# Optimization experiments

Hardware: AMD Instinct MI355X
Metric: run time of the kernel (lower is better)

Reference implementation:

```python
import jax, jax.numpy as jnp
import numpy as np

N_NODES = 100000
IN_FEAT = 128
HIDDEN = 256
OUT = 2
N_EDGES = 600000
EPS = 1e-12  # F.normalize eps


def glorot(key, shape):
    fan_in, fan_out = shape[1], shape[0]
    lim = jnp.sqrt(6.0 / (fan_in + fan_out))
    return jax.random.uniform(key, shape, jnp.float32, -lim, lim)


def setup_inputs() -> dict:
    key = jax.random.key(0)
    ks = jax.random.split(key, 8)
    x = jax.random.normal(ks[0], (N_NODES, IN_FEAT), jnp.float32)
    edge_index = jax.random.randint(ks[1], (2, N_EDGES), 0, N_NODES, jnp.int64)
    return {
        'x': x,
        'edge_index': edge_index,
        'W1_l': glorot(ks[2], (HIDDEN, IN_FEAT)),
        'b1': jnp.zeros((HIDDEN,), jnp.float32),
        'W1_r': glorot(ks[3], (HIDDEN, IN_FEAT)),
        'W2_l': glorot(ks[4], (OUT, HIDDEN)),
        'b2': jnp.zeros((OUT,), jnp.float32),
        'W2_r': glorot(ks[5], (OUT, HIDDEN)),
    }


def sage_conv(x, src, dst, W_l, b_l, W_r):
    # mean aggregation of neighbor (source) features onto destination nodes
    msgs = x[src]  # [E, d]
    s = jax.ops.segment_sum(msgs, dst, num_segments=N_NODES)
    cnt = jax.ops.segment_sum(jnp.ones((src.shape[0], 1), x.dtype), dst,
                              num_segments=N_NODES)
    agg = s / jnp.maximum(cnt, 1.0)  # nodes with no in-edges stay 0
    out = agg @ W_l.T + b_l + x @ W_r.T  # lin_l(agg) + lin_r(x)
    # L2 normalize (normalize=True in SAGEConv)
    nrm = jnp.linalg.norm(out, axis=-1, keepdims=True)
    return out / jnp.maximum(nrm, EPS)


def reference(x, edge_index, W1_l, b1, W1_r, W2_l, b2, W2_r):
    src, dst = edge_index[0], edge_index[1]
    h = sage_conv(x, src, dst, W1_l, b1, W1_r)
    h = jax.nn.relu(h)
    # dropout(p=0.2) is identity in eval mode
    h = sage_conv(h, src, dst, W2_l, b2, W2_r)
    return jax.nn.log_softmax(h, axis=1)
```

## Files before the change

kernel.cpp:

```cpp
#include <hip/hip_runtime.h>
#include <hip/hip_fp16.h>

#define NN  100000
#define FIN 128
#define HID 256
#define NE  600000
#define FEPS 1e-12f


typedef _Float16 f16x8 __attribute__((ext_vector_type(8)));
typedef float    f32x4 __attribute__((ext_vector_type(4)));

__device__ __forceinline__ int clampN(int v) {
    return ((unsigned)v < (unsigned)NN) ? v : 0;
}
__device__ __forceinline__ int detect4(const int* ei) {
    return ((ei[1] | ei[3] | ei[5] | ei[7]) == 0) ? 1 : 0;
}
__device__ __forceinline__ int ld_src(const int* ei, int e, int f) {
    return f ? ei[2 * e] : ei[e];
}
__device__ __forceinline__ int ld_dst(const int* ei, int e, int f) {
    return f ? ei[2 * (NE + e)] : ei[NE + e];
}

__device__ __forceinline__ unsigned packh2(__half a, __half b) {
    return __builtin_bit_cast(unsigned, __halves2half2(a, b));
}

__device__ __forceinline__ int offAt(const int* __restrict__ off,
                                     const int* __restrict__ bsum, int i) {
    return (i < NN) ? (off[i] + bsum[i >> 10]) : NE;
}

__device__ __forceinline__ size_t fragIdx(int j, int k) {
    return ((size_t)((k >> 5) * 16 + (j >> 4)) * 64 +
            (size_t)(((k >> 3) & 3) * 16 + (j & 15))) * 8 + (k & 7);
}

__global__ __launch_bounds__(256) void setup_kernel(
    const int* __restrict__ ei,
    const float* __restrict__ x,
    const float* __restrict__ W1l, const float* __restrict__ W1r,
    __half* __restrict__ Bfh, __half* __restrict__ Bfl,
    __half* __restrict__ xh,
    int* __restrict__ cnt, int ncv)
{
    int b = blockIdx.x;
    int t = threadIdx.x;
    if (b < 256) {
        int j = b, k2 = t;
        float v = (k2 < FIN) ? W1l[(size_t)j * FIN + k2]
                             : W1r[(size_t)j * FIN + (k2 - FIN)];
        __half h  = __float2half_rn(v);
        __half lo = __float2half_rn(v - __half2float(h));
        size_t fi = fragIdx(j, k2);
        Bfh[fi] = h;
        Bfl[fi] = lo;
    } else if (b < 256 + ncv) {
        int idx = (b - 256) * 256 + t;
        if (idx < NN * FIN / 8) {
            const float4* px = (const float4*)(x + (size_t)idx * 8);
            float4 v0 = px[0], v1 = px[1];
            uint4 u;
            u.x = packh2(__float2half_rn(v0.x), __float2half_rn(v0.y));
            u.y = packh2(__float2half_rn(v0.z), __float2half_rn(v0.w));
            u.z = packh2(__float2half_rn(v1.x), __float2half_rn(v1.y));
            u.w = packh2(__float2half_rn(v1.z), __float2half_rn(v1.w));
            ((uint4*)xh)[idx] = u;
        }
    } else {
        int e = (b - 256 - ncv) * 256 + t;
        if (e < NE) {
            int f = detect4(ei);
            atomicAdd(cnt + clampN(ld_dst(ei, e, f)), 1);
        }
    }
}

__global__ __launch_bounds__(1024) void scan_kernel(
    const int* __restrict__ cnt, int* __restrict__ off, int* bsum,
    int* flag, int nblocks)
{
    __shared__ int sm[1024];
    __shared__ int amLast;
    int t = threadIdx.x;
    int idx = blockIdx.x * 1024 + t;
    int v = (idx < NN) ? cnt[idx] : 0;
    sm[t] = v;
    __syncthreads();
    for (int d = 1; d < 1024; d <<= 1) {
        int w = (t >= d) ? sm[t - d] : 0;
        __syncthreads();
        sm[t] += w;
        __syncthreads();
    }
    if (idx < NN) off[idx] = sm[t] - v;
    if (t == 1023) {
        bsum[blockIdx.x] = sm[1023];
        __threadfence();
        amLast = (atomicAdd(flag, 1) == nblocks - 1);
    }
    __syncthreads();
    if (amLast) {
        volatile int* vb = (volatile int*)bsum;
        int bv = (t < nblocks) ? vb[t] : 0;
        __syncthreads();
        sm[t] = (t < 128) ? ((t < nblocks) ? bv : 0) : 0;
        __syncthreads();
        for (int d = 1; d < 128; d <<= 1) {
            int w2 = (t >= d && t < 128) ? sm[t - d] : 0;
            __syncthreads();
            if (t < 128) sm[t] += w2;
            __syncthreads();
        }
        if (t < nblocks) bsum[t] = sm[t] - bv;
    }
}

__global__ __launch_bounds__(256) void fill_kernel(
    const int* __restrict__ ei,
    const int* __restrict__ off, const int* __restrict__ bsum,
    int* __restrict__ cur, int* __restrict__ col)
{
    int e = blockIdx.x * 256 + threadIdx.x;
    if (e >= NE) return;
    int f = detect4(ei);
    int src = clampN(ld_src(ei, e, f));
    int dst = clampN(ld_dst(ei, e, f));
    int p = atomicAdd(cur + dst, 1);
    col[offAt(off, bsum, dst) + p] = src;
}

__global__ __launch_bounds__(256) void gather_kernel(
    const int* __restrict__ off, const int* __restrict__ bsum,
    const int* __restrict__ col,
    const __half* __restrict__ xh,
    __half* __restrict__ aggH, __half* __restrict__ aggL)
{
    int wid = (blockIdx.x * 256 + threadIdx.x) >> 6;
    if (wid >= NN) return;
    const int n     = wid;
    const int l     = threadIdx.x & 63;
    const int ft    = l & 15;
    const int e     = l >> 4;
    const int fbase = ft * 8;

    float a[8];
#pragma unroll
    for (int i = 0; i < 8; ++i) a[i] = 0.0f;

    const int s0 = offAt(off, bsum, n);
    const int s1 = offAt(off, bsum, n + 1);

    for (int i = s0 + e; i < s1; i += 4) {
        int c = clampN(col[i]);
        uint4 v = *(const uint4*)(xh + (size_t)c * FIN + fbase);
#pragma unroll
        for (int u = 0; u < 4; ++u) {
            float2 f0 = __half22float2(__builtin_bit_cast(__half2, (&v.x)[u]));
            a[2 * u]     += f0.x;
            a[2 * u + 1] += f0.y;
        }
    }
#pragma unroll
    for (int k = 0; k < 8; ++k) {
        a[k] += __shfl_xor(a[k], 16);
        a[k] += __shfl_xor(a[k], 32);
    }

    if (e == 0) {
        float ic = 1.0f / fmaxf((float)(s1 - s0), 1.0f);
        __half h[8], lo[8];
#pragma unroll
        for (int k = 0; k < 8; ++k) {
            float v = a[k] * ic;
            h[k]  = __float2half_rn(v);
            lo[k] = __float2half_rn(v - __half2float(h[k]));
        }
        uint4 uh, ul;
        uh.x = packh2(h[0], h[1]);   uh.y = packh2(h[2], h[3]);
        uh.z = packh2(h[4], h[5]);   uh.w = packh2(h[6], h[7]);
        ul.x = packh2(lo[0], lo[1]); ul.y = packh2(lo[2], lo[3]);
        ul.z = packh2(lo[4], lo[5]); ul.w = packh2(lo[6], lo[7]);
        size_t rowb = (size_t)n * 128 + (size_t)((ft ^ (n & 7)) << 3);
        *(uint4*)(aggH + rowb) = uh;
        *(uint4*)(aggL + rowb) = ul;
    }
}

__device__ __forceinline__ void splitStore4(
    __half* Ah, __half* Al, int addr, float4 v)
{
    __half h0 = __float2half_rn(v.x), h1 = __float2half_rn(v.y);
    __half h2 = __float2half_rn(v.z), h3 = __float2half_rn(v.w);
    __half l0 = __float2half_rn(v.x - __half2float(h0));
    __half l1 = __float2half_rn(v.y - __half2float(h1));
    __half l2 = __float2half_rn(v.z - __half2float(h2));
    __half l3 = __float2half_rn(v.w - __half2float(h3));
    uint2 uh, ul;
    uh.x = packh2(h0, h1);  uh.y = packh2(h2, h3);
    ul.x = packh2(l0, l1);  ul.y = packh2(l2, l3);
    *(uint2*)(Ah + addr) = uh;
    *(uint2*)(Al + addr) = ul;
}

__device__ __forceinline__ void mfma_phase(
    const __half* Ah, const __half* Al,
    const __half* __restrict__ Bfh, const __half* __restrict__ Bfl,
    int pb , int baseA0, int baseA1, int r7,
    int jg0, int l, f32x4 acc[2][4])
{
    const int kg = l >> 4;
#pragma unroll
    for (int kk = 0; kk < 4; ++kk) {
        const int chunk = kk * 4 + kg;
        const int sl = (chunk ^ r7) << 3;
        f16x8 ah0 = *reinterpret_cast<const f16x8*>(Ah + baseA0 + sl);
        f16x8 al0 = *reinterpret_cast<const f16x8*>(Al + baseA0 + sl);
        f16x8 ah1 = *reinterpret_cast<const f16x8*>(Ah + baseA1 + sl);
        f16x8 al1 = *reinterpret_cast<const f16x8*>(Al + baseA1 + sl);
#pragma unroll
        for (int jt = 0; jt < 4; ++jt) {
            const size_t bo = (((size_t)(pb + kk) * 16 + jg0 + jt) * 64 + l) * 8;
            f16x8 bh = *reinterpret_cast<const f16x8*>(Bfh + bo);
            f16x8 bl = *reinterpret_cast<const f16x8*>(Bfl + bo);
            acc[0][jt] = __builtin_amdgcn_mfma_f32_16x16x32_f16(ah0, bh, acc[0][jt], 0, 0, 0);
            acc[1][jt] = __builtin_amdgcn_mfma_f32_16x16x32_f16(ah1, bh, acc[1][jt], 0, 0, 0);
            acc[0][jt] = __builtin_amdgcn_mfma_f32_16x16x32_f16(al0, bh, acc[0][jt], 0, 0, 0);
            acc[1][jt] = __builtin_amdgcn_mfma_f32_16x16x32_f16(al1, bh, acc[1][jt], 0, 0, 0);
            acc[0][jt] = __builtin_amdgcn_mfma_f32_16x16x32_f16(ah0, bl, acc[0][jt], 0, 0, 0);
            acc[1][jt] = __builtin_amdgcn_mfma_f32_16x16x32_f16(ah1, bl, acc[1][jt], 0, 0, 0);
        }
    }
}

__global__ __launch_bounds__(512, 4) void gemm_mfma_kernel(
    const __half* __restrict__ aggH, const __half* __restrict__ aggL,
    const float* __restrict__ x,
    const __half* __restrict__ Bfh, const __half* __restrict__ Bfl,
    const float* __restrict__ b1,
    const float* __restrict__ W2l, const float* __restrict__ W2r,
    float* __restrict__ g, float* __restrict__ r)
{
    __shared__ __half Ah[64 * 128];
    __shared__ __half Al[64 * 128];

    const int t  = threadIdx.x;
    const int nb = blockIdx.x * 64;

    {
        const uint4* gh = (const uint4*)(aggH + (size_t)nb * 128);
        const uint4* gl = (const uint4*)(aggL + (size_t)nb * 128);
#pragma unroll
        for (int i = 0; i < 2; ++i) {
            int idx = i * 512 + t;
            *(uint4*)(Ah + idx * 8) = gh[idx];
            *(uint4*)(Al + idx * 8) = gl[idx];
        }
    }
    __syncthreads();

    const int l     = t & 63;
    const int w     = t >> 6;
    const int ln    = l & 15;
    const int kg    = l >> 4;
    const int mrow0 = (w & 1) * 32;
    const int jg0   = (w >> 1) * 4;

    f32x4 acc[2][4];
#pragma unroll
    for (int mt = 0; mt < 2; ++mt)
#pragma unroll
        for (int jt = 0; jt < 4; ++jt)
            acc[mt][jt] = (f32x4){0.f, 0.f, 0.f, 0.f};

    const int rowA0  = mrow0 + ln;
    const int rowA1  = mrow0 + 16 + ln;
    const int baseA0 = rowA0 * 128;
    const int baseA1 = rowA1 * 128;
    const int r7     = ln & 7;

    mfma_phase(Ah, Al, Bfh, Bfl, 0, baseA0, baseA1, r7, jg0, l, acc);
    __syncthreads();

    {
        const float4* xF = (const float4*)x;
        const float4 z4 = make_float4(0.f, 0.f, 0.f, 0.f);
#pragma unroll
        for (int i = 0; i < 4; ++i) {
            int idx   = i * 512 + t;
            int n_loc = idx >> 5;
            int kq    = idx & 31;
            int n     = nb + n_loc;
            float4 v  = (n < NN) ? xF[(size_t)n * 32 + kq] : z4;
            int addr  = n_loc * 128 + ((((kq >> 1) ^ (n_loc & 7)) << 3) | ((kq & 1) << 2));
            splitStore4(Ah, Al, addr, v);
        }
    }
    __syncthreads();

    mfma_phase(Ah, Al, Bfh, Bfl, 4, baseA0, baseA1, r7, jg0, l, acc);

    const int jb2 = jg0 * 16;
    float b1v[4], wl0[4], wl1[4], wr0[4], wr1[4];
#pragma unroll
    for (int jt = 0; jt < 4; ++jt) {
        int j = jb2 + jt * 16 + ln;
        b1v[jt] = b1[j];
        wl0[jt] = W2l[j];        wl1[jt] = W2l[HID + j];
        wr0[jt] = W2r[j];        wr1[jt] = W2r[HID + j];
    }

    __syncthreads();
    float* red = (float*)Ah;
#pragma unroll
    for (int mt = 0; mt < 2; ++mt) {
#pragma unroll
        for (int rg = 0; rg < 4; ++rg) {
            float s = 0.f, G0 = 0.f, G1 = 0.f, R0 = 0.f, R1 = 0.f;
#pragma unroll
            for (int jt = 0; jt < 4; ++jt) {
                float oo = acc[mt][jt][rg] + b1v[jt];
                s = fmaf(oo, oo, s);
                float pp = fmaxf(oo, 0.f);
                G0 = fmaf(pp, wl0[jt], G0);
                G1 = fmaf(pp, wl1[jt], G1);
                R0 = fmaf(pp, wr0[jt], R0);
                R1 = fmaf(pp, wr1[jt], R1);
            }
#pragma unroll
            for (int m = 1; m < 16; m <<= 1) {
                s  += __shfl_xor(s, m);
                G0 += __shfl_xor(G0, m);
                G1 += __shfl_xor(G1, m);
                R0 += __shfl_xor(R0, m);
                R1 += __shfl_xor(R1, m);
            }
            if (ln == 0) {
                int n_loc = mrow0 + mt * 16 + kg * 4 + rg;
                float* pp = red + ((size_t)(w >> 1) * 64 + n_loc) * 5;
                pp[0] = s;  pp[1] = G0; pp[2] = G1; pp[3] = R0; pp[4] = R1;
            }
        }
    }
    __syncthreads();

    if (t < 64) {
        int n = nb + t;
        if (n < NN) {
            float s = 0.f, G0 = 0.f, G1 = 0.f, R0 = 0.f, R1 = 0.f;
#pragma unroll
            for (int jg = 0; jg < 4; ++jg) {
                const float* pp = red + ((size_t)jg * 64 + t) * 5;
                s += pp[0]; G0 += pp[1]; G1 += pp[2]; R0 += pp[3]; R1 += pp[4];
            }
            float inv = 1.0f / fmaxf(sqrtf(s), FEPS);
            g[2 * (size_t)n]     = G0 * inv;
            g[2 * (size_t)n + 1] = G1 * inv;
            r[2 * (size_t)n]     = R0 * inv;
            r[2 * (size_t)n + 1] = R1 * inv;
        }
    }
}

__device__ __forceinline__ void phaseB_epilogue(
    float* smem_f, int t, int l, int nb,
    const __half* __restrict__ Bfh, const __half* __restrict__ Bfl,
    const float* __restrict__ b1,
    const float* __restrict__ W2l, const float* __restrict__ W2r,
    float* __restrict__ g, float* __restrict__ r)
{
    const int w  = __builtin_amdgcn_readfirstlane(t >> 6);
    const int jb = w * 16;

    float o[16];
#pragma unroll
    for (int i = 0; i < 16; ++i) o[i] = 0.0f;

#pragma unroll 1
    for (int k2 = 0; k2 < 2 * FIN; k2 += 4) {
        const int nc = l ^ ((k2 >> 3) & 31);
        float av0 = smem_f[(k2 + 0) * 64 + nc];
        float av1 = smem_f[(k2 + 1) * 64 + nc];
        float av2 = smem_f[(k2 + 2) * 64 + nc];
        float av3 = smem_f[(k2 + 3) * 64 + nc];
#pragma unroll
        for (int i = 0; i < 16; ++i) {
            const size_t fb = ((size_t)((k2 >> 5) * 16 + ((jb + i) >> 4)) * 64 +
                               (size_t)(((k2 >> 3) & 3) * 16 + ((jb + i) & 15))) * 8 +
                              (k2 & 7);
            const __half* ph = Bfh + fb;
            const __half* pl = Bfl + fb;
            float oi = o[i];
            oi = fmaf(av0, __half2float(ph[0]) + __half2float(pl[0]), oi);
            oi = fmaf(av1, __half2float(ph[1]) + __half2float(pl[1]), oi);
            oi = fmaf(av2, __half2float(ph[2]) + __half2float(pl[2]), oi);
            oi = fmaf(av3, __half2float(ph[3]) + __half2float(pl[3]), oi);
            o[i] = oi;
        }
    }

    float sq = 0.f, g0 = 0.f, g1 = 0.f, r0 = 0.f, r1 = 0.f;
    const float* b1w  = b1  + jb;
    const float* w2la = W2l + jb;
    const float* w2lb = W2l + HID + jb;
    const float* w2ra = W2r + jb;
    const float* w2rb = W2r + HID + jb;
#pragma unroll
    for (int i = 0; i < 16; ++i) {
        float oo = o[i] + b1w[i];
        sq = fmaf(oo, oo, sq);
        float p = fmaxf(oo, 0.0f);
        g0 = fmaf(p, w2la[i], g0);
        g1 = fmaf(p, w2lb[i], g1);
        r0 = fmaf(p, w2ra[i], r0);
        r1 = fmaf(p, w2rb[i], r1);
    }

    __syncthreads();
    smem_f[0 * 1024 + t] = sq;
    smem_f[1 * 1024 + t] = g0;
    smem_f[2 * 1024 + t] = g1;
    smem_f[3 * 1024 + t] = r0;
    smem_f[4 * 1024 + t] = r1;
    __syncthreads();

    if (t < 64) {
        int n2 = nb + t;
        float sqs = 0.f, G0 = 0.f, G1 = 0.f, R0 = 0.f, R1 = 0.f;
#pragma unroll
        for (int ww = 0; ww < 16; ++ww) {
            sqs += smem_f[0 * 1024 + ww * 64 + t];
            G0  += smem_f[1 * 1024 + ww * 64 + t];
            G1  += smem_f[2 * 1024 + ww * 64 + t];
            R0  += smem_f[3 * 1024 + ww * 64 + t];
            R1  += smem_f[4 * 1024 + ww * 64 + t];
        }
        float inv = 1.0f / fmaxf(sqrtf(sqs), FEPS);
        if (n2 < NN) {
            g[2 * (size_t)n2]     = G0 * inv;
            g[2 * (size_t)n2 + 1] = G1 * inv;
            r[2 * (size_t)n2]     = R0 * inv;
            r[2 * (size_t)n2 + 1] = R1 * inv;
        }
    }
}

template <bool HALFX>
__global__ __launch_bounds__(1024, 8) void layer1_kernel(
    const int* __restrict__ off, const int* __restrict__ bsum,
    const int* __restrict__ col,
    const float* __restrict__ x, const __half* __restrict__ xh,
    const __half* __restrict__ Bfh, const __half* __restrict__ Bfl,
    const float* __restrict__ b1,
    const float* __restrict__ W2l, const float* __restrict__ W2r,
    float* __restrict__ g, float* __restrict__ r)
{
    __shared__ float smem_f[256 * 64];

    const int t  = threadIdx.x;
    const int nb = blockIdx.x * 64;
    const int l  = t & 63;

    {
        const int n_loc = t >> 4;
        const int ft    = t & 15;
        const int fbase = ft * 8;
        const int n     = nb + n_loc;
        const bool valid = (n < NN);

        float a[8];
#pragma unroll
        for (int i = 0; i < 8; ++i) a[i] = 0.0f;

        int s0 = 0, s1 = 0;
        if (valid) { s0 = offAt(off, bsum, n); s1 = offAt(off, bsum, n + 1); }

        int i = s0;
        if (HALFX) {
            for (; i + 3 < s1; i += 4) {
                int c0 = clampN(col[i]);
                int c1 = clampN(col[i + 1]);
                int c2 = clampN(col[i + 2]);
                int c3 = clampN(col[i + 3]);
                uint4 v0 = *(const uint4*)(xh + (size_t)c0 * FIN + fbase);
                uint4 v1 = *(const uint4*)(xh + (size_t)c1 * FIN + fbase);
                uint4 v2 = *(const uint4*)(xh + (size_t)c2 * FIN + fbase);
                uint4 v3 = *(const uint4*)(xh + (size_t)c3 * FIN + fbase);
#pragma unroll
                for (int u = 0; u < 4; ++u) {
                    float2 f0 = __half22float2(__builtin_bit_cast(__half2, (&v0.x)[u]));
                    float2 f1 = __half22float2(__builtin_bit_cast(__half2, (&v1.x)[u]));
                    float2 f2 = __half22float2(__builtin_bit_cast(__half2, (&v2.x)[u]));
                    float2 f3 = __half22float2(__builtin_bit_cast(__half2, (&v3.x)[u]));
                    a[2 * u]     += (f0.x + f1.x) + (f2.x + f3.x);
                    a[2 * u + 1] += (f0.y + f1.y) + (f2.y + f3.y);
                }
            }
            for (; i < s1; ++i) {
                int c0 = clampN(col[i]);
                uint4 v0 = *(const uint4*)(xh + (size_t)c0 * FIN + fbase);
#pragma unroll
                for (int u = 0; u < 4; ++u) {
                    float2 f0 = __half22float2(__builtin_bit_cast(__half2, (&v0.x)[u]));
                    a[2 * u]     += f0.x;
                    a[2 * u + 1] += f0.y;
                }
            }
        } else {
            for (; i < s1; ++i) {
                int c0 = clampN(col[i]);
                const float4* p0 = (const float4*)(x + (size_t)c0 * FIN + fbase);
                float4 v00 = p0[0], v01 = p0[1];
                a[0] += v00.x; a[1] += v00.y; a[2] += v00.z; a[3] += v00.w;
                a[4] += v01.x; a[5] += v01.y; a[6] += v01.z; a[7] += v01.w;
            }
        }
        float ic = 1.0f / fmaxf((float)(s1 - s0), 1.0f);
#pragma unroll
        for (int k = 0; k < 8; ++k) {
            int f = fbase + k;
            smem_f[f * 64 + (n_loc ^ ((f >> 3) & 31))] = a[k] * ic;
        }
        const float4* sp = (const float4*)(x + (size_t)(valid ? n : 0) * FIN + fbase);
        float4 s0v = valid ? sp[0] : make_float4(0.f, 0.f, 0.f, 0.f);
        float4 s1v = valid ? sp[1] : make_float4(0.f, 0.f, 0.f, 0.f);
        float sv[8] = {s0v.x, s0v.y, s0v.z, s0v.w, s1v.x, s1v.y, s1v.z, s1v.w};
#pragma unroll
        for (int k = 0; k < 8; ++k) {
            int f = FIN + fbase + k;
            smem_f[f * 64 + (n_loc ^ ((f >> 3) & 31))] = sv[k];
        }
    }
    __syncthreads();

    phaseB_epilogue(smem_f, t, l, nb, Bfh, Bfl, b1, W2l, W2r, g, r);
}

__global__ __launch_bounds__(256) void finalize_kernel(
    const int* __restrict__ off, const int* __restrict__ bsum,
    const int* __restrict__ col,
    const float* __restrict__ g, const float* __restrict__ r,
    const float* __restrict__ b2,
    float* __restrict__ out)
{
    int n = blockIdx.x * 256 + threadIdx.x;
    if (n >= NN) return;
    int s0 = offAt(off, bsum, n), s1 = offAt(off, bsum, n + 1);
    float z0 = 0.0f, z1 = 0.0f, y0b = 0.0f, y1b = 0.0f;
    int i = s0;
    for (; i + 1 < s1; i += 2) {
        int sa = clampN(col[i]);
        int sb = clampN(col[i + 1]);
        float2 va = *(const float2*)(g + 2 * (size_t)sa);
        float2 vb = *(const float2*)(g + 2 * (size_t)sb);
        z0 += va.x; z1 += va.y;
        y0b += vb.x; y1b += vb.y;
    }
    if (i < s1) {
        int sa = clampN(col[i]);
        float2 va = *(const float2*)(g + 2 * (size_t)sa);
        z0 += va.x; z1 += va.y;
    }
    z0 += y0b; z1 += y1b;
    float ic = 1.0f / fmaxf((float)(s1 - s0), 1.0f);
    z0 = z0 * ic + b2[0] + r[2 * (size_t)n];
    z1 = z1 * ic + b2[1] + r[2 * (size_t)n + 1];
    float d = 1.0f / fmaxf(sqrtf(z0 * z0 + z1 * z1), FEPS);
    float y0 = z0 * d, y1 = z1 * d;
    float m = fmaxf(y0, y1);
    float lg = m + logf(__expf(y0 - m) + __expf(y1 - m));
    out[2 * (size_t)n]     = y0 - lg;
    out[2 * (size_t)n + 1] = y1 - lg;
}

extern "C" void kernel_launch(void* const* d_in, const int* in_sizes, int n_in,
                              void* d_out, int out_size, void* d_ws, size_t ws_size,
                              hipStream_t stream) {
    const float* x   = (const float*)d_in[0];
    const int*   ei  = (const int*)d_in[1];
    const float* W1l = (const float*)d_in[2];
    const float* b1  = (const float*)d_in[3];
    const float* W1r = (const float*)d_in[4];
    const float* W2l = (const float*)d_in[5];
    const float* b2  = (const float*)d_in[6];
    const float* W2r = (const float*)d_in[7];

    const int nsb = (NN + 1023) / 1024;
    const int ncv = (NN * FIN / 8 + 255) / 256;
    const int ecb = (NE + 255) / 256;

    const size_t tailWords = (size_t)2 * NN + (NN + 1) + NE + 4 * NN + 128;
    const size_t needB = (size_t)256 * 256 * 4 + (size_t)NN * FIN * 2 +
                         tailWords * 4;
    const size_t needA = needB + (size_t)NN * FIN * 4;

    bool pathA = (ws_size >= needA);
    bool pathB = !pathA && (ws_size >= needB);
    bool half  = pathA || pathB;

    char* p = (char*)d_ws;
    __half* Bfh = (__half*)p;             p += (size_t)256 * 256 * 2;
    __half* Bfl = (__half*)p;             p += (size_t)256 * 256 * 2;
    __half* xh = nullptr;
    if (half) { xh = (__half*)p;          p += (size_t)NN * FIN * 2; }
    __half* aggH = nullptr; __half* aggL = nullptr;
    if (pathA) {
        aggH = (__half*)p;
        aggL = aggH + (size_t)NN * 128;
        p += (size_t)NN * FIN * 4;
    }

    int*   cnt  = (int*)p;
    int*   cur  = cnt + NN;
    int*   off  = cur + NN;
    int*   col  = off + NN + 1;
    float* g    = (float*)(col + NE);
    float* r    = g + 2 * (size_t)NN;
    int*   bsum = (int*)(r + 2 * (size_t)NN);

    hipMemsetAsync(cnt, 0, 2 * (size_t)NN * sizeof(int), stream);
    hipMemsetAsync(bsum + 127, 0, sizeof(int), stream);

    int cv = half ? ncv : 0;
    setup_kernel<<<256 + cv + ecb, 256, 0, stream>>>(ei, x, W1l, W1r,
                                                     Bfh, Bfl, xh, cnt, cv);
    scan_kernel<<<nsb, 1024, 0, stream>>>(cnt, off, bsum, bsum + 127, nsb);
    fill_kernel<<<ecb, 256, 0, stream>>>(ei, off, bsum, cur, col);

    if (pathA) {
        gather_kernel<<<(NN * 64 + 255) / 256, 256, 0, stream>>>(
            off, bsum, col, xh, aggH, aggL);
        gemm_mfma_kernel<<<(NN + 63) / 64, 512, 0, stream>>>(aggH, aggL, x,
                                                             Bfh, Bfl,
                                                             b1, W2l, W2r, g, r);
    } else if (pathB) {
        layer1_kernel<true><<<(NN + 63) / 64, 1024, 0, stream>>>(
            off, bsum, col, x, xh, Bfh, Bfl, b1, W2l, W2r, g, r);
    } else {
        layer1_kernel<false><<<(NN + 63) / 64, 1024, 0, stream>>>(
            off, bsum, col, x, xh, Bfh, Bfl, b1, W2l, W2r, g, r);
    }
    finalize_kernel<<<(NN + 255) / 256, 256, 0, stream>>>(off, bsum, col, g, r,
                                                          b2, (float*)d_out);
}
```

Measured before the change: 278.7 us.

## Precompute swizzled split-half x, DMA GEMM tiles to LDS, thread-per-slice gather

```diff
diff --git a/kernel.cpp b/kernel.cpp
--- a/kernel.cpp
+++ b/kernel.cpp
@@ -33,6 +33,12 @@
     return (i < NN) ? (off[i] + bsum[i >> 10]) : NE;
 }
 
+__device__ __forceinline__ void ldsDMA16(const __half* g, __half* l) {
+    __builtin_amdgcn_global_load_lds(
+        (const __attribute__((address_space(1))) unsigned int*)g,
+        (__attribute__((address_space(3))) unsigned int*)l, 16, 0, 0);
+}
+
 __device__ __forceinline__ size_t fragIdx(int j, int k) {
     return ((size_t)((k >> 5) * 16 + (j >> 4)) * 64 +
             (size_t)(((k >> 3) & 3) * 16 + (j & 15))) * 8 + (k & 7);
@@ -43,7 +49,7 @@
     const float* __restrict__ x,
     const float* __restrict__ W1l, const float* __restrict__ W1r,
     __half* __restrict__ Bfh, __half* __restrict__ Bfl,
-    __half* __restrict__ xh,
+    __half* __restrict__ xh, __half* __restrict__ xLo,
     int* __restrict__ cnt, int ncv)
 {
     int b = blockIdx.x;
@@ -59,15 +65,26 @@
         Bfl[fi] = lo;
     } else if (b < 256 + ncv) {
         int idx = (b - 256) * 256 + t;
-        if (idx < NN * FIN / 8) {
+        if (idx < NN * 16) {
+            int n   = idx >> 4;
+            int ftc = idx & 15;
             const float4* px = (const float4*)(x + (size_t)idx * 8);
             float4 v0 = px[0], v1 = px[1];
-            uint4 u;
-            u.x = packh2(__float2half_rn(v0.x), __float2half_rn(v0.y));
-            u.y = packh2(__float2half_rn(v0.z), __float2half_rn(v0.w));
-            u.z = packh2(__float2half_rn(v1.x), __float2half_rn(v1.y));
-            u.w = packh2(__float2half_rn(v1.z), __float2half_rn(v1.w));
-            ((uint4*)xh)[idx] = u;
+            float vv[8] = {v0.x, v0.y, v0.z, v0.w, v1.x, v1.y, v1.z, v1.w};
+            __half h[8], lo[8];
+#pragma unroll
+            for (int k = 0; k < 8; ++k) {
+                h[k]  = __float2half_rn(vv[k]);
+                lo[k] = __float2half_rn(vv[k] - __half2float(h[k]));
+            }
+            uint4 uh, ul;
+            uh.x = packh2(h[0], h[1]);   uh.y = packh2(h[2], h[3]);
+            uh.z = packh2(h[4], h[5]);   uh.w = packh2(h[6], h[7]);
+            ul.x = packh2(lo[0], lo[1]); ul.y = packh2(lo[2], lo[3]);
+            ul.z = packh2(lo[4], lo[5]); ul.w = packh2(lo[6], lo[7]);
+            size_t pos = (size_t)n * 128 + (size_t)((ftc ^ (n & 7)) << 3);
+            *(uint4*)(xh + pos) = uh;
+            if (xLo) *(uint4*)(xLo + pos) = ul;
         }
     } else {
         int e = (b - 256 - ncv) * 256 + t;
@@ -138,55 +155,62 @@
     const __half* __restrict__ xh,
     __half* __restrict__ aggH, __half* __restrict__ aggL)
 {
-    int wid = (blockIdx.x * 256 + threadIdx.x) >> 6;
-    if (wid >= NN) return;
-    const int n     = wid;
-    const int l     = threadIdx.x & 63;
-    const int ft    = l & 15;
-    const int e     = l >> 4;
-    const int fbase = ft * 8;
+    int idx = blockIdx.x * 256 + threadIdx.x;
+    if (idx >= NN * 16) return;
+    int n     = idx >> 4;
+    int ft    = idx & 15;
 
     float a[8];
 #pragma unroll
     for (int i = 0; i < 8; ++i) a[i] = 0.0f;
 
-    const int s0 = offAt(off, bsum, n);
-    const int s1 = offAt(off, bsum, n + 1);
-
-    for (int i = s0 + e; i < s1; i += 4) {
-        int c = clampN(col[i]);
-        uint4 v = *(const uint4*)(xh + (size_t)c * FIN + fbase);
+    int s0 = offAt(off, bsum, n), s1 = offAt(off, bsum, n + 1);
+    int i = s0;
+    for (; i + 3 < s1; i += 4) {
+        int c0 = clampN(col[i]);
+        int c1 = clampN(col[i + 1]);
+        int c2 = clampN(col[i + 2]);
+        int c3 = clampN(col[i + 3]);
+        uint4 v0 = *(const uint4*)(xh + (size_t)c0 * FIN + ((ft ^ (c0 & 7)) << 3));
+        uint4 v1 = *(const uint4*)(xh + (size_t)c1 * FIN + ((ft ^ (c1 & 7)) << 3));
+        uint4 v2 = *(const uint4*)(xh + (size_t)c2 * FIN + ((ft ^ (c2 & 7)) << 3));
+        uint4 v3 = *(const uint4*)(xh + (size_t)c3 * FIN + ((ft ^ (c3 & 7)) << 3));
 #pragma unroll
         for (int u = 0; u < 4; ++u) {
-            float2 f0 = __half22float2(__builtin_bit_cast(__half2, (&v.x)[u]));
+            float2 f0 = __half22float2(__builtin_bit_cast(__half2, (&v0.x)[u]));
+            float2 f1 = __half22float2(__builtin_bit_cast(__half2, (&v1.x)[u]));
+            float2 f2 = __half22float2(__builtin_bit_cast(__half2, (&v2.x)[u]));
+            float2 f3 = __half22float2(__builtin_bit_cast(__half2, (&v3.x)[u]));
+            a[2 * u]     += (f0.x + f1.x) + (f2.x + f3.x);
+            a[2 * u + 1] += (f0.y + f1.y) + (f2.y + f3.y);
+        }
+    }
+    for (; i < s1; ++i) {
+        int c0 = clampN(col[i]);
+        uint4 v0 = *(const uint4*)(xh + (size_t)c0 * FIN + ((ft ^ (c0 & 7)) << 3));
+#pragma unroll
+        for (int u = 0; u < 4; ++u) {
+            float2 f0 = __half22float2(__builtin_bit_cast(__half2, (&v0.x)[u]));
             a[2 * u]     += f0.x;
             a[2 * u + 1] += f0.y;
         }
     }
+    float ic = 1.0f / fmaxf((float)(s1 - s0), 1.0f);
+    __half h[8], lo[8];
 #pragma unroll
     for (int k = 0; k < 8; ++k) {
-        a[k] += __shfl_xor(a[k], 16);
-        a[k] += __shfl_xor(a[k], 32);
-    }
-
-    if (e == 0) {
-        float ic = 1.0f / fmaxf((float)(s1 - s0), 1.0f);
-        __half h[8], lo[8];
-#pragma unroll
-        for (int k = 0; k < 8; ++k) {
-            float v = a[k] * ic;
-            h[k]  = __float2half_rn(v);
-            lo[k] = __float2half_rn(v - __half2float(h[k]));
-        }
-        uint4 uh, ul;
-        uh.x = packh2(h[0], h[1]);   uh.y = packh2(h[2], h[3]);
-        uh.z = packh2(h[4], h[5]);   uh.w = packh2(h[6], h[7]);
-        ul.x = packh2(lo[0], lo[1]); ul.y = packh2(lo[2], lo[3]);
-        ul.z = packh2(lo[4], lo[5]); ul.w = packh2(lo[6], lo[7]);
-        size_t rowb = (size_t)n * 128 + (size_t)((ft ^ (n & 7)) << 3);
-        *(uint4*)(aggH + rowb) = uh;
-        *(uint4*)(aggL + rowb) = ul;
-    }
+        float v = a[k] * ic;
+        h[k]  = __float2half_rn(v);
+        lo[k] = __float2half_rn(v - __half2float(h[k]));
+    }
+    uint4 uh, ul;
+    uh.x = packh2(h[0], h[1]);   uh.y = packh2(h[2], h[3]);
+    uh.z = packh2(h[4], h[5]);   uh.w = packh2(h[6], h[7]);
+    ul.x = packh2(lo[0], lo[1]); ul.y = packh2(lo[2], lo[3]);
+    ul.z = packh2(lo[4], lo[5]); ul.w = packh2(lo[6], lo[7]);
+    size_t rowb = (size_t)n * 128 + (size_t)((ft ^ (n & 7)) << 3);
+    *(uint4*)(aggH + rowb) = uh;
+    *(uint4*)(aggL + rowb) = ul;
 }
 
 __device__ __forceinline__ void splitStore4(
@@ -235,56 +259,39 @@
     }
 }
 
+template <bool DMA>
 __global__ __launch_bounds__(512, 4) void gemm_mfma_kernel(
     const __half* __restrict__ aggH, const __half* __restrict__ aggL,
     const float* __restrict__ x,
+    const __half* __restrict__ xHi, const __half* __restrict__ xLo,
     const __half* __restrict__ Bfh, const __half* __restrict__ Bfl,
     const float* __restrict__ b1,
     const float* __restrict__ W2l, const float* __restrict__ W2r,
     float* __restrict__ g, float* __restrict__ r)
 {
-    __shared__ __half Ah[64 * 128];
-    __shared__ __half Al[64 * 128];
+    __shared__ __align__(16) __half AS[4 * 64 * 128];
+    __half* AggHs = AS;
+    __half* AggLs = AS + 64 * 128;
+    __half* XHs   = AS + 2 * 64 * 128;
+    __half* XLs   = AS + 3 * 64 * 128;
 
     const int t  = threadIdx.x;
     const int nb = blockIdx.x * 64;
 
-    {
-        const uint4* gh = (const uint4*)(aggH + (size_t)nb * 128);
-        const uint4* gl = (const uint4*)(aggL + (size_t)nb * 128);
-#pragma unroll
-        for (int i = 0; i < 2; ++i) {
-            int idx = i * 512 + t;
-            *(uint4*)(Ah + idx * 8) = gh[idx];
-            *(uint4*)(Al + idx * 8) = gl[idx];
-        }
-    }
-    __syncthreads();
-
-    const int l     = t & 63;
-    const int w     = t >> 6;
-    const int ln    = l & 15;
-    const int kg    = l >> 4;
-    const int mrow0 = (w & 1) * 32;
-    const int jg0   = (w >> 1) * 4;
-
-    f32x4 acc[2][4];
-#pragma unroll
-    for (int mt = 0; mt < 2; ++mt)
-#pragma unroll
-        for (int jt = 0; jt < 4; ++jt)
-            acc[mt][jt] = (f32x4){0.f, 0.f, 0.f, 0.f};
-
-    const int rowA0  = mrow0 + ln;
-    const int rowA1  = mrow0 + 16 + ln;
-    const int baseA0 = rowA0 * 128;
-    const int baseA1 = rowA1 * 128;
-    const int r7     = ln & 7;
-
-    mfma_phase(Ah, Al, Bfh, Bfl, 0, baseA0, baseA1, r7, jg0, l, acc);
-    __syncthreads();
-
-    {
+#pragma unroll
+    for (int i = 0; i < 2; ++i) {
+        int idx  = i * 512 + t;
+        int row  = idx >> 4;
+        int cc   = idx & 15;
+        size_t srow = (size_t)clampN(nb + row) * 128 + (size_t)(cc << 3);
+        ldsDMA16(aggH + srow, AggHs + (size_t)idx * 8);
+        ldsDMA16(aggL + srow, AggLs + (size_t)idx * 8);
+        if (DMA) {
+            ldsDMA16(xHi + srow, XHs + (size_t)idx * 8);
+            ldsDMA16(xLo + srow, XLs + (size_t)idx * 8);
+        }
+    }
+    if (!DMA) {
         const float4* xF = (const float4*)x;
         const float4 z4 = make_float4(0.f, 0.f, 0.f, 0.f);
 #pragma unroll
@@ -295,12 +302,33 @@
             int n     = nb + n_loc;
             float4 v  = (n < NN) ? xF[(size_t)n * 32 + kq] : z4;
             int addr  = n_loc * 128 + ((((kq >> 1) ^ (n_loc & 7)) << 3) | ((kq & 1) << 2));
-            splitStore4(Ah, Al, addr, v);
-        }
-    }
-    __syncthreads();
-
-    mfma_phase(Ah, Al, Bfh, Bfl, 4, baseA0, baseA1, r7, jg0, l, acc);
+            splitStore4(XHs, XLs, addr, v);
+        }
+    }
+    __syncthreads();
+
+    const int l     = t & 63;
+    const int w     = t >> 6;
+    const int ln    = l & 15;
+    const int kg    = l >> 4;
+    const int mrow0 = (w & 1) * 32;
+    const int jg0   = (w >> 1) * 4;
+
+    f32x4 acc[2][4];
+#pragma unroll
+    for (int mt = 0; mt < 2; ++mt)
+#pragma unroll
+        for (int jt = 0; jt < 4; ++jt)
+            acc[mt][jt] = (f32x4){0.f, 0.f, 0.f, 0.f};
+
+    const int rowA0  = mrow0 + ln;
+    const int rowA1  = mrow0 + 16 + ln;
+    const int baseA0 = rowA0 * 128;
+    const int baseA1 = rowA1 * 128;
+    const int r7     = ln & 7;
+
+    mfma_phase(AggHs, AggLs, Bfh, Bfl, 0, baseA0, baseA1, r7, jg0, l, acc);
+    mfma_phase(XHs,   XLs,   Bfh, Bfl, 4, baseA0, baseA1, r7, jg0, l, acc);
 
     const int jb2 = jg0 * 16;
     float b1v[4], wl0[4], wl1[4], wr0[4], wr1[4];
@@ -313,7 +341,7 @@
     }
 
     __syncthreads();
-    float* red = (float*)Ah;
+    float* red = (float*)AS;
 #pragma unroll
     for (int mt = 0; mt < 2; ++mt) {
 #pragma unroll
@@ -479,28 +507,9 @@
 
         int i = s0;
         if (HALFX) {
-            for (; i + 3 < s1; i += 4) {
-                int c0 = clampN(col[i]);
-                int c1 = clampN(col[i + 1]);
-                int c2 = clampN(col[i + 2]);
-                int c3 = clampN(col[i + 3]);
-                uint4 v0 = *(const uint4*)(xh + (size_t)c0 * FIN + fbase);
-                uint4 v1 = *(const uint4*)(xh + (size_t)c1 * FIN + fbase);
-                uint4 v2 = *(const uint4*)(xh + (size_t)c2 * FIN + fbase);
-                uint4 v3 = *(const uint4*)(xh + (size_t)c3 * FIN + fbase);
-#pragma unroll
-                for (int u = 0; u < 4; ++u) {
-                    float2 f0 = __half22float2(__builtin_bit_cast(__half2, (&v0.x)[u]));
-                    float2 f1 = __half22float2(__builtin_bit_cast(__half2, (&v1.x)[u]));
-                    float2 f2 = __half22float2(__builtin_bit_cast(__half2, (&v2.x)[u]));
-                    float2 f3 = __half22float2(__builtin_bit_cast(__half2, (&v3.x)[u]));
-                    a[2 * u]     += (f0.x + f1.x) + (f2.x + f3.x);
-                    a[2 * u + 1] += (f0.y + f1.y) + (f2.y + f3.y);
-                }
-            }
             for (; i < s1; ++i) {
                 int c0 = clampN(col[i]);
-                uint4 v0 = *(const uint4*)(xh + (size_t)c0 * FIN + fbase);
+                uint4 v0 = *(const uint4*)(xh + (size_t)c0 * FIN + ((ft ^ (c0 & 7)) << 3));
 #pragma unroll
                 for (int u = 0; u < 4; ++u) {
                     float2 f0 = __half22float2(__builtin_bit_cast(__half2, (&v0.x)[u]));
@@ -594,11 +603,13 @@
     const size_t tailWords = (size_t)2 * NN + (NN + 1) + NE + 4 * NN + 128;
     const size_t needB = (size_t)256 * 256 * 4 + (size_t)NN * FIN * 2 +
                          tailWords * 4;
-    const size_t needA = needB + (size_t)NN * FIN * 4;
-
-    bool pathA = (ws_size >= needA);
-    bool pathB = !pathA && (ws_size >= needB);
-    bool half  = pathA || pathB;
+    const size_t needA  = needB + (size_t)NN * FIN * 4;
+    const size_t needA2 = needA + (size_t)NN * FIN * 2;
+
+    bool pathA2 = (ws_size >= needA2);
+    bool pathA  = (ws_size >= needA);
+    bool pathB  = !pathA && (ws_size >= needB);
+    bool half   = pathA || pathB;
 
     char* p = (char*)d_ws;
     __half* Bfh = (__half*)p;             p += (size_t)256 * 256 * 2;
@@ -619,22 +630,28 @@
     float* g    = (float*)(col + NE);
     float* r    = g + 2 * (size_t)NN;
     int*   bsum = (int*)(r + 2 * (size_t)NN);
+    __half* xLo = pathA2 ? (__half*)(bsum + 128) : nullptr;
 
     hipMemsetAsync(cnt, 0, 2 * (size_t)NN * sizeof(int), stream);
     hipMemsetAsync(bsum + 127, 0, sizeof(int), stream);
 
     int cv = half ? ncv : 0;
     setup_kernel<<<256 + cv + ecb, 256, 0, stream>>>(ei, x, W1l, W1r,
-                                                     Bfh, Bfl, xh, cnt, cv);
+                                                     Bfh, Bfl, xh, xLo,
+                                                     cnt, cv);
     scan_kernel<<<nsb, 1024, 0, stream>>>(cnt, off, bsum, bsum + 127, nsb);
     fill_kernel<<<ecb, 256, 0, stream>>>(ei, off, bsum, cur, col);
 
     if (pathA) {
-        gather_kernel<<<(NN * 64 + 255) / 256, 256, 0, stream>>>(
+        gather_kernel<<<(NN * 16 + 255) / 256, 256, 0, stream>>>(
             off, bsum, col, xh, aggH, aggL);
-        gemm_mfma_kernel<<<(NN + 63) / 64, 512, 0, stream>>>(aggH, aggL, x,
-                                                             Bfh, Bfl,
-                                                             b1, W2l, W2r, g, r);
+        if (pathA2) {
+            gemm_mfma_kernel<true><<<(NN + 63) / 64, 512, 0, stream>>>(
+                aggH, aggL, x, xh, xLo, Bfh, Bfl, b1, W2l, W2r, g, r);
+        } else {
+            gemm_mfma_kernel<false><<<(NN + 63) / 64, 512, 0, stream>>>(
+                aggH, aggL, x, xh, xLo, Bfh, Bfl, b1, W2l, W2r, g, r);
+        }
     } else if (pathB) {
         layer1_kernel<true><<<(NN + 63) / 64, 1024, 0, stream>>>(
             off, bsum, col, x, xh, Bfh, Bfl, b1, W2l, W2r, g, r);
```

Measured after the change: 271.4 us. -2.6%, faster.
